# Kernel tuning notes

Measured on AMD Instinct MI355X. Metric: run time of the kernel, lower is better.

## Reference

```python
import jax, jax.numpy as jnp
import numpy as np

B, S, D = 1, 2048, 4096
H, KVH, HD = 32, 8, 128


def setup_inputs() -> dict:
    key = jax.random.key(0)
    ks = jax.random.split(key, 6)
    x = jax.random.normal(ks[0], (B, S, D), dtype=jnp.float32)
    # Llama3 RoPE angles: theta = 500000
    inv_freq = 1.0 / (500000.0 ** (np.arange(0, HD, 2, dtype=np.float32) / HD))
    ang = np.arange(S, dtype=np.float32)[:, None] * inv_freq[None, :]  # [S, HD//2]
    freqs_cos = jnp.asarray(np.cos(ang), dtype=jnp.float32)
    freqs_sin = jnp.asarray(np.sin(ang), dtype=jnp.float32)
    sc = 0.02
    wq = jax.random.normal(ks[1], (H * HD, D), dtype=jnp.float32) * sc
    wk = jax.random.normal(ks[2], (KVH * HD, D), dtype=jnp.float32) * sc
    wv = jax.random.normal(ks[3], (KVH * HD, D), dtype=jnp.float32) * sc
    wo = jax.random.normal(ks[4], (D, H * HD), dtype=jnp.float32) * sc
    return {"x": x, "freqs_cos": freqs_cos, "freqs_sin": freqs_sin,
            "wq": wq, "wk": wk, "wv": wv, "wo": wo}


def _rope(t, cos, sin):
    # t: [B, S, h, HD]; rotate consecutive pairs (complex multiply)
    t2 = t.reshape(*t.shape[:-1], HD // 2, 2)
    x0, x1 = t2[..., 0], t2[..., 1]
    c = cos[None, :, None, :]
    s = sin[None, :, None, :]
    r0 = x0 * c - x1 * s
    r1 = x0 * s + x1 * c
    return jnp.stack([r0, r1], axis=-1).reshape(t.shape)


def reference(x, freqs_cos, freqs_sin, wq, wk, wv, wo):
    b, s, _ = x.shape
    q = jnp.einsum('bsd,ed->bse', x, wq).reshape(b, s, H, HD)
    k = jnp.einsum('bsd,ed->bse', x, wk).reshape(b, s, KVH, HD)
    v = jnp.einsum('bsd,ed->bse', x, wv).reshape(b, s, KVH, HD)
    q = _rope(q, freqs_cos, freqs_sin)
    k = _rope(k, freqs_cos, freqs_sin)
    # GQA: repeat kv heads
    rep = H // KVH
    k = jnp.repeat(k, rep, axis=2)
    v = jnp.repeat(v, rep, axis=2)
    scale = 1.0 / jnp.sqrt(jnp.asarray(HD, dtype=x.dtype))
    scores = jnp.einsum('bqhd,bkhd->bhqk', q, k) * scale
    causal = jnp.tril(jnp.ones((s, s), dtype=bool))
    scores = jnp.where(causal[None, None], scores, jnp.finfo(scores.dtype).min)
    p = jax.nn.softmax(scores, axis=-1)
    out = jnp.einsum('bhqk,bkhd->bqhd', p, v).reshape(b, s, H * HD)
    return jnp.einsum('bse,de->bsd', out, wo)
```

## Files before the change

kernel.cpp:

```cpp
#include <hip/hip_runtime.h>

typedef unsigned short u16;
typedef short bf16x8 __attribute__((ext_vector_type(8)));
typedef float f32x4 __attribute__((ext_vector_type(4)));

#define S_LEN 2048
#define ATT_SCALE (0.08838834764831845f * 1.4426950408889634f)
#define NEG_BIG  -1.0e30f

static __device__ __forceinline__ float bf2f(u16 u) {
  union { unsigned int i; float f; } v; v.i = ((unsigned int)u) << 16; return v.f;
}
static __device__ __forceinline__ u16 f2bf(float f) {
  union { float f; unsigned int i; } v; v.f = f;
  unsigned int x = v.i;
  return (u16)((x + 0x7fffu + ((x >> 16) & 1u)) >> 16);
}
static __device__ __forceinline__ float fexp2(float x) {
  return __builtin_amdgcn_exp2f(x);
}

static __device__ __forceinline__ void gl_lds16(const u16* g, u16* l) {
  __builtin_amdgcn_global_load_lds(
      (const __attribute__((address_space(1))) unsigned int*)g,
      (__attribute__((address_space(3))) unsigned int*)l, 16, 0, 0);
}

static __device__ __forceinline__ bf16x8 load8(const u16* p) { return *(const bf16x8*)p; }
static __device__ __forceinline__ bf16x8 load8(const float* p) {
  f32x4 a = *(const f32x4*)p;
  f32x4 b = *(const f32x4*)(p + 4);
  bf16x8 r;
  r[0] = (short)f2bf(a[0]); r[1] = (short)f2bf(a[1]);
  r[2] = (short)f2bf(a[2]); r[3] = (short)f2bf(a[3]);
  r[4] = (short)f2bf(b[0]); r[5] = (short)f2bf(b[1]);
  r[6] = (short)f2bf(b[2]); r[7] = (short)f2bf(b[3]);
  return r;
}
static __device__ __forceinline__ void store_out(u16* C, size_t i, float v)  { C[i] = f2bf(v); }
static __device__ __forceinline__ void store_out(float* C, size_t i, float v){ C[i] = v; }

__global__ __launch_bounds__(256) void f2b_kernel(
    const float* __restrict__ s, u16* __restrict__ d, int n8) {
  int i = blockIdx.x * 256 + threadIdx.x;
  if (i >= n8) return;
  *(bf16x8*)&d[(size_t)i * 8] = load8(s + (size_t)i * 8);
}

template <typename OT>
static __device__ __forceinline__ void gemm_core(
    const u16* __restrict__ A, const u16* __restrict__ B, OT* __restrict__ C,
    int K, int ldc, int bm, int bn) {
  __shared__ __align__(16) u16 As[128 * 64];
  __shared__ __align__(16) u16 Bs[128 * 64];
  const int tid  = threadIdx.x;
  const int lane = tid & 63;
  const int wave = tid >> 6;
  const int wm = (wave >> 1) << 6;
  const int wn = (wave & 1) << 6;
  const int col  = lane & 15;
  const int quad = lane >> 4;

  const f32x4 fzero = {0.f, 0.f, 0.f, 0.f};
  f32x4 acc[4][4];
#pragma unroll
  for (int i = 0; i < 4; ++i)
#pragma unroll
    for (int j = 0; j < 4; ++j) acc[i][j] = fzero;

  const int srow = (lane >> 3);
  const int sc8  = lane & 7;

  for (int k0 = 0; k0 < K; k0 += 64) {
#pragma unroll
    for (int i = 0; i < 4; ++i) {
      int r = wave * 32 + i * 8 + srow;
      int src = (sc8 ^ (r & 7)) << 3;
      gl_lds16(A + (size_t)(bm + r) * K + k0 + src, &As[(wave * 32 + i * 8) * 64]);
      gl_lds16(B + (size_t)(bn + r) * K + k0 + src, &Bs[(wave * 32 + i * 8) * 64]);
    }
    __syncthreads();
#pragma unroll
    for (int kk = 0; kk < 64; kk += 32) {
      bf16x8 af[4], bfr[4];
#pragma unroll
      for (int mt = 0; mt < 4; ++mt) {
        int row = wm + mt * 16 + col;
        af[mt] = *(const bf16x8*)&As[row * 64 + ((((kk >> 3) + quad) ^ (col & 7)) << 3)];
      }
#pragma unroll
      for (int nt = 0; nt < 4; ++nt) {
        int row = wn + nt * 16 + col;
        bfr[nt] = *(const bf16x8*)&Bs[row * 64 + ((((kk >> 3) + quad) ^ (col & 7)) << 3)];
      }
#pragma unroll
      for (int mt = 0; mt < 4; ++mt)
#pragma unroll
        for (int nt = 0; nt < 4; ++nt)
          acc[mt][nt] = __builtin_amdgcn_mfma_f32_16x16x32_bf16(
              af[mt], bfr[nt], acc[mt][nt], 0, 0, 0);
    }
    __syncthreads();
  }
#pragma unroll
  for (int mt = 0; mt < 4; ++mt)
#pragma unroll
    for (int nt = 0; nt < 4; ++nt)
#pragma unroll
      for (int r = 0; r < 4; ++r) {
        int row = bm + wm + mt * 16 + quad * 4 + r;
        int cn  = bn + wn + nt * 16 + col;
        store_out(C, (size_t)row * ldc + cn, acc[mt][nt][r]);
      }
}

__global__ __launch_bounds__(256) void gemm_qkv(
    const u16* __restrict__ xb, const u16* __restrict__ wqb,
    const u16* __restrict__ wkb, const u16* __restrict__ wvb,
    u16* __restrict__ q, u16* __restrict__ k, u16* __restrict__ v) {
  int bx = blockIdx.x;
  const u16* B; u16* C; int ldc, bn;
  if (bx < 32)      { B = wqb; C = q; ldc = 4096; bn = bx * 128; }
  else if (bx < 40) { B = wkb; C = k; ldc = 1024; bn = (bx - 32) * 128; }
  else              { B = wvb; C = v; ldc = 1024; bn = (bx - 40) * 128; }
  gemm_core<u16>(xb, B, C, 4096, ldc, blockIdx.y * 128, bn);
}

__global__ __launch_bounds__(256) void gemm_o(
    const u16* __restrict__ ao, const u16* __restrict__ wob, float* __restrict__ out) {
  gemm_core<float>(ao, wob, out, 4096, 4096, blockIdx.y * 128, blockIdx.x * 128);
}

#define LDK 72
template <typename AT, typename BT, typename OT>
__global__ __launch_bounds__(256) void gemm_bt(
    const AT* __restrict__ A, const BT* __restrict__ B,
    OT* __restrict__ C, int M, int N, int K) {
  __shared__ __align__(16) u16 As[128 * LDK];
  __shared__ __align__(16) u16 Bs[128 * LDK];
  const int tid  = threadIdx.x;
  const int lane = tid & 63;
  const int wave = tid >> 6;
  const int wm = (wave >> 1) << 6;
  const int wn = (wave & 1) << 6;
  const int col  = lane & 15;
  const int quad = lane >> 4;
  const int bm = blockIdx.y * 128;
  const int bn = blockIdx.x * 128;

  const f32x4 fzero = {0.f, 0.f, 0.f, 0.f};
  f32x4 acc[4][4];
#pragma unroll
  for (int i = 0; i < 4; ++i)
#pragma unroll
    for (int j = 0; j < 4; ++j) acc[i][j] = fzero;

  const int sr = tid >> 3;
  const int sc = (tid & 7) * 8;
  const AT* Aptr = A + (size_t)(bm + sr) * K + sc;
  const BT* Bptr = B + (size_t)(bn + sr) * K + sc;

  for (int k0 = 0; k0 < K; k0 += 64) {
#pragma unroll
    for (int p = 0; p < 4; ++p) {
      *(bf16x8*)&As[(sr + 32 * p) * LDK + sc] = load8(Aptr + (size_t)(32 * p) * K + k0);
      *(bf16x8*)&Bs[(sr + 32 * p) * LDK + sc] = load8(Bptr + (size_t)(32 * p) * K + k0);
    }
    __syncthreads();
#pragma unroll
    for (int kk = 0; kk < 64; kk += 32) {
      bf16x8 af[4], bfr[4];
#pragma unroll
      for (int mt = 0; mt < 4; ++mt)
        af[mt] = *(const bf16x8*)&As[(wm + mt * 16 + col) * LDK + kk + quad * 8];
#pragma unroll
      for (int nt = 0; nt < 4; ++nt)
        bfr[nt] = *(const bf16x8*)&Bs[(wn + nt * 16 + col) * LDK + kk + quad * 8];
#pragma unroll
      for (int mt = 0; mt < 4; ++mt)
#pragma unroll
        for (int nt = 0; nt < 4; ++nt)
          acc[mt][nt] = __builtin_amdgcn_mfma_f32_16x16x32_bf16(
              af[mt], bfr[nt], acc[mt][nt], 0, 0, 0);
    }
    __syncthreads();
  }
#pragma unroll
  for (int mt = 0; mt < 4; ++mt)
#pragma unroll
    for (int nt = 0; nt < 4; ++nt)
#pragma unroll
      for (int r = 0; r < 4; ++r) {
        int row = bm + wm + mt * 16 + quad * 4 + r;
        int cn  = bn + wn + nt * 16 + col;
        store_out(C, (size_t)row * N + cn, acc[mt][nt][r]);
      }
}

__global__ __launch_bounds__(256) void rope_kernel(
    u16* __restrict__ q, u16* __restrict__ k,
    const float* __restrict__ cs, const float* __restrict__ sn) {
  int idx = blockIdx.x * 256 + threadIdx.x;
  const int QP = S_LEN * 32 * 64;
  u16* base;
  int s, i;
  bool isq = idx < QP;
  if (isq) {
    s = idx >> 11; int w = idx & 2047; i = w & 63;
    base = q + (size_t)s * 4096 + (w >> 6) * 128 + 2 * i;
  } else {
    int j = idx - QP;
    s = j >> 9; int w = j & 511; i = w & 63;
    base = k + (size_t)s * 1024 + (w >> 6) * 128 + 2 * i;
  }
  float c  = cs[s * 64 + i];
  float sv = sn[s * 64 + i];
  float x0 = bf2f(base[0]);
  float x1 = bf2f(base[1]);
  float r0 = x0 * c - x1 * sv;
  float r1 = x0 * sv + x1 * c;
  if (isq) { r0 *= ATT_SCALE; r1 *= ATT_SCALE; }
  base[0] = f2bf(r0);
  base[1] = f2bf(r1);
}

__global__ __launch_bounds__(512, 4) void attn_kernel(
    const u16* __restrict__ Q, const u16* __restrict__ K,
    const u16* __restrict__ V, u16* __restrict__ O) {
  const int ib   = blockIdx.x;
  const int h    = blockIdx.y;
  const int kvh  = h >> 2;
  const int tid  = threadIdx.x;
  const int lane = tid & 63;
  const int wave = tid >> 6;
  const int grp  = wave >> 2;
  const int wl   = wave & 3;
  const int col  = lane & 15;
  const int quad = lane >> 4;
  const int gt   = tid & 255;

  __shared__ __align__(16) u16 SMEM[2][16384];
  u16* Kb = &SMEM[grp][0];
  u16* Vb = &SMEM[grp][8192];

  const f32x4 fzero = {0.f, 0.f, 0.f, 0.f};

  const int krow = lane >> 4;
  const int kcnk = lane & 15;
  const int vsc  = (gt & 15) * 8;
  const int vrp  = gt >> 4;
  const int vrot = gt & 7;

  for (int t = 0; t < 2; ++t) {
    const int qb   = t ? 31 - ib : ib;
    const int qpos = qb * 64 + wl * 16 + col;
    const int ql   = wl * 16 + col;

    bf16x8 qf[4];
#pragma unroll
    for (int kb = 0; kb < 4; ++kb)
      qf[kb] = *(const bf16x8*)&Q[(size_t)qpos * 4096 + h * 128 + kb * 32 + quad * 8];

    f32x4 oacc[8];
#pragma unroll
    for (int nt = 0; nt < 8; ++nt) oacc[nt] = fzero;
    float m_ = NEG_BIG, l_ = 0.f;

    const int n  = qb + 1;
    const int h0 = (n + 1) >> 1;
    const int c0 = grp ? h0 : 0;
    const int c1 = grp ? n  : h0;

    for (int rnd = 0; rnd < h0; ++rnd) {
      const int c = c0 + rnd;
      const bool act = c < c1;
      if (act) {
        const int pos0 = c * 64;
#pragma unroll
        for (int i = 0; i < 4; ++i) {
          int r = wl * 16 + i * 4 + krow;
          int src = ((kcnk & 8) | ((kcnk ^ r) & 7)) << 3;
          gl_lds16(&K[(size_t)(pos0 + r) * 1024 + kvh * 128 + src],
                   &Kb[(wl * 16 + i * 4) * 128]);
        }
#pragma unroll
        for (int it = 0; it < 2; ++it) {
          int rp = vrp + it * 16;
          const u16* vp = &V[(size_t)(pos0 + 2 * rp) * 1024 + kvh * 128 + vsc];
          union { bf16x8 v; u16 u[8]; } ue, uo;
          ue.v = *(const bf16x8*)vp;
          uo.v = *(const bf16x8*)(vp + 1024);
          int pc = rp >> 2, pi = rp & 3;
#pragma unroll
          for (int j = 0; j < 8; ++j) {
            int jj = (j + vrot) & 7;
            int hd = vsc + jj;
            unsigned val = (unsigned)ue.u[jj] | ((unsigned)uo.u[jj] << 16);
            *(unsigned*)&Vb[hd * 64 + ((pc ^ (hd & 7)) << 3) + pi * 2] = val;
          }
        }
      }
      __syncthreads();
      if (act) {
        const int pos0 = c * 64;
        const bool diag = (c == qb);

        f32x4 sv[4];
#pragma unroll
        for (int kv = 0; kv < 4; ++kv) sv[kv] = fzero;
        __builtin_amdgcn_s_setprio(1);
#pragma unroll
        for (int kv = 0; kv < 4; ++kv) {
          int r = kv * 16 + col;
#pragma unroll
          for (int kb = 0; kb < 4; ++kb) {
            int kq = kb * 4 + quad;
            int slot = (kq & 8) | ((kq ^ r) & 7);
            bf16x8 kf = *(const bf16x8*)&Kb[r * 128 + slot * 8];
            sv[kv] = __builtin_amdgcn_mfma_f32_16x16x32_bf16(kf, qf[kb], sv[kv], 0, 0, 0);
          }
        }
        __builtin_amdgcn_s_setprio(0);

        float mx = NEG_BIG;
        if (diag) {
#pragma unroll
          for (int kv = 0; kv < 4; ++kv)
#pragma unroll
            for (int r = 0; r < 4; ++r) {
              float s = (pos0 + kv * 16 + quad * 4 + r) <= qpos ? sv[kv][r] : NEG_BIG;
              sv[kv][r] = s;
              mx = fmaxf(mx, s);
            }
        } else {
#pragma unroll
          for (int kv = 0; kv < 4; ++kv)
#pragma unroll
            for (int r = 0; r < 4; ++r) mx = fmaxf(mx, sv[kv][r]);
        }
        mx = fmaxf(mx, __shfl_xor(mx, 16));
        mx = fmaxf(mx, __shfl_xor(mx, 32));
        if (!__all(mx - m_ <= 8.f)) {
          float mnew  = fmaxf(m_, mx);
          float alpha = fexp2(m_ - mnew);
          l_ *= alpha;
#pragma unroll
          for (int nt = 0; nt < 8; ++nt) {
            oacc[nt][0] *= alpha; oacc[nt][1] *= alpha;
            oacc[nt][2] *= alpha; oacc[nt][3] *= alpha;
          }
          m_ = mnew;
        }
        float ls = 0.f;
#pragma unroll
        for (int kv = 0; kv < 4; ++kv)
#pragma unroll
          for (int r = 0; r < 4; ++r) {
            float p = fexp2(sv[kv][r] - m_);
            sv[kv][r] = p;
            ls += p;
          }
        ls += __shfl_xor(ls, 16);
        ls += __shfl_xor(ls, 32);
        l_ += ls;

        unsigned pk[4][2];
#pragma unroll
        for (int kv = 0; kv < 4; ++kv) {
          pk[kv][0] = (unsigned)f2bf(sv[kv][0]) | ((unsigned)f2bf(sv[kv][1]) << 16);
          pk[kv][1] = (unsigned)f2bf(sv[kv][2]) | ((unsigned)f2bf(sv[kv][3]) << 16);
        }

        const int idxA = col + 16 * (2 * (quad & 1));
        const int idxB = idxA + 16;
        const bool hi  = quad >= 2;
#pragma unroll
        for (int kc = 0; kc < 2; ++kc) {
          unsigned a00 = __shfl(pk[2 * kc][0],     idxA);
          unsigned a01 = __shfl(pk[2 * kc][1],     idxA);
          unsigned a10 = __shfl(pk[2 * kc + 1][0], idxA);
          unsigned a11 = __shfl(pk[2 * kc + 1][1], idxA);
          unsigned b00 = __shfl(pk[2 * kc][0],     idxB);
          unsigned b01 = __shfl(pk[2 * kc][1],     idxB);
          unsigned b10 = __shfl(pk[2 * kc + 1][0], idxB);
          unsigned b11 = __shfl(pk[2 * kc + 1][1], idxB);
          union { unsigned u[4]; bf16x8 v; } pb;
          pb.u[0] = hi ? a10 : a00;
          pb.u[1] = hi ? a11 : a01;
          pb.u[2] = hi ? b10 : b00;
          pb.u[3] = hi ? b11 : b01;
          __builtin_amdgcn_s_setprio(1);
#pragma unroll
          for (int nt = 0; nt < 8; ++nt) {
            int hd = nt * 16 + col;
            int pc = kc * 4 + quad;
            bf16x8 vf = *(const bf16x8*)&Vb[hd * 64 + ((pc ^ (hd & 7)) << 3)];
            oacc[nt] = __builtin_amdgcn_mfma_f32_16x16x32_bf16(vf, pb.v, oacc[nt], 0, 0, 0);
          }
          __builtin_amdgcn_s_setprio(0);
        }
      }
      __syncthreads();
    }

    float* MF = (float*)&SMEM[0][0];
    float* ML = MF + 64 * 132;
    if (grp == 1) {
#pragma unroll
      for (int nt = 0; nt < 8; ++nt)
        *(f32x4*)&MF[ql * 132 + nt * 16 + quad * 4] = oacc[nt];
      if (quad == 0) { ML[2 * ql] = m_; ML[2 * ql + 1] = l_; }
    }
    __syncthreads();
    if (grp == 0) {
      float m1 = ML[2 * ql], l1 = ML[2 * ql + 1];
      float mn = fmaxf(m_, m1);
      float a0 = fexp2(m_ - mn), a1 = fexp2(m1 - mn);
      float li = 1.f / (l_ * a0 + l1 * a1);
      a0 *= li; a1 *= li;
#pragma unroll
      for (int nt = 0; nt < 8; ++nt) {
        f32x4 o1 = *(const f32x4*)&MF[ql * 132 + nt * 16 + quad * 4];
        union { u16 u[4]; unsigned long long ll; } w;
        w.u[0] = f2bf(oacc[nt][0] * a0 + o1[0] * a1);
        w.u[1] = f2bf(oacc[nt][1] * a0 + o1[1] * a1);
        w.u[2] = f2bf(oacc[nt][2] * a0 + o1[2] * a1);
        w.u[3] = f2bf(oacc[nt][3] * a0 + o1[3] * a1);
        *(unsigned long long*)&O[(size_t)qpos * 4096 + h * 128 + nt * 16 + quad * 4] = w.ll;
      }
    }
    __syncthreads();
  }
}

extern "C" void kernel_launch(void* const* d_in, const int* in_sizes, int n_in,
                              void* d_out, int out_size, void* d_ws, size_t ws_size,
                              hipStream_t stream) {
  const float* x  = (const float*)d_in[0];
  const float* fc = (const float*)d_in[1];
  const float* fs = (const float*)d_in[2];
  const float* wq = (const float*)d_in[3];
  const float* wk = (const float*)d_in[4];
  const float* wv = (const float*)d_in[5];
  const float* wo = (const float*)d_in[6];
  float* out = (float*)d_out;

  u16* q  = (u16*)d_ws;
  u16* k  = q + (size_t)8388608;
  u16* v  = k + (size_t)2097152;
  u16* ao = v + (size_t)2097152;

  dim3 blk(256, 1, 1);
  dim3 ablk(512, 1, 1);
  const size_t NEED_FAST = 109051904ULL;

  if (ws_size >= NEED_FAST) {
    u16* xb  = ao  + (size_t)8388608;
    u16* wqb = xb  + (size_t)8388608;
    u16* wkb = wqb + (size_t)16777216;
    u16* wvb = wkb + (size_t)4194304;
    u16* wob = wqb;

    hipLaunchKernelGGL(f2b_kernel, dim3(4096, 1, 1), blk, 0, stream, x,  xb,  1048576);
    hipLaunchKernelGGL(f2b_kernel, dim3(8192, 1, 1), blk, 0, stream, wq, wqb, 2097152);
    hipLaunchKernelGGL(f2b_kernel, dim3(2048, 1, 1), blk, 0, stream, wk, wkb, 524288);
    hipLaunchKernelGGL(f2b_kernel, dim3(2048, 1, 1), blk, 0, stream, wv, wvb, 524288);
    hipLaunchKernelGGL(gemm_qkv, dim3(48, 16, 1), blk, 0, stream, xb, wqb, wkb, wvb, q, k, v);
    hipLaunchKernelGGL(f2b_kernel, dim3(8192, 1, 1), blk, 0, stream, wo, wob, 2097152);
    hipLaunchKernelGGL(rope_kernel, dim3(20480, 1, 1), blk, 0, stream, q, k, fc, fs);
    hipLaunchKernelGGL(attn_kernel, dim3(16, 32, 1), ablk, 0, stream, q, k, v, ao);
    hipLaunchKernelGGL(gemm_o, dim3(32, 16, 1), blk, 0, stream, ao, wob, out);
  } else {
    hipLaunchKernelGGL((gemm_bt<float, float, u16>), dim3(32, 16, 1), blk, 0, stream,
                       x, wq, q, 2048, 4096, 4096);
    hipLaunchKernelGGL((gemm_bt<float, float, u16>), dim3(8, 16, 1),  blk, 0, stream,
                       x, wk, k, 2048, 1024, 4096);
    hipLaunchKernelGGL((gemm_bt<float, float, u16>), dim3(8, 16, 1),  blk, 0, stream,
                       x, wv, v, 2048, 1024, 4096);
    hipLaunchKernelGGL(rope_kernel, dim3(20480, 1, 1), blk, 0, stream, q, k, fc, fs);
    hipLaunchKernelGGL(attn_kernel, dim3(16, 32, 1), ablk, 0, stream, q, k, v, ao);
    hipLaunchKernelGGL((gemm_bt<u16, float, float>), dim3(32, 16, 1), blk, 0, stream,
                       ao, wo, out, 2048, 4096, 4096);
  }
}
```

Before: 542.4 us.

## Enlarge attention query tile to 128 rows per block with two subtiles per wave

Each attention block now handles 128 query rows, with each wave holding two 16-row query subtiles, so every K/V fragment loaded from LDS feeds two MFMAs. The grid halves to 8x32 and the two wave groups split the key range evenly, which removes the idle inactive rounds of the old uneven split. The LDS swizzle is changed and a separate stat buffer is added for the merge step. The aim is to cut LDS traffic and K/V reloads per FLOP, at the cost of doubled accumulator registers (launch bounds lowered to 2), fewer blocks, and masking applied to more tiles.

```diff
diff --git a/kernel.cpp b/kernel.cpp
--- a/kernel.cpp
+++ b/kernel.cpp
@@ -224,7 +224,7 @@
   base[1] = f2bf(r1);
 }
 
-__global__ __launch_bounds__(512, 4) void attn_kernel(
+__global__ __launch_bounds__(512, 2) void attn_kernel(
     const u16* __restrict__ Q, const u16* __restrict__ K,
     const u16* __restrict__ V, u16* __restrict__ O) {
   const int ib   = blockIdx.x;
@@ -237,9 +237,11 @@
   const int wl   = wave & 3;
   const int col  = lane & 15;
   const int quad = lane >> 4;
+  const int chd  = col >> 3;
   const int gt   = tid & 255;
 
   __shared__ __align__(16) u16 SMEM[2][16384];
+  __shared__ float MLS[256];
   u16* Kb = &SMEM[grp][0];
   u16* Vb = &SMEM[grp][8192];
 
@@ -252,181 +254,213 @@
   const int vrot = gt & 7;
 
   for (int t = 0; t < 2; ++t) {
-    const int qb   = t ? 31 - ib : ib;
-    const int qpos = qb * 64 + wl * 16 + col;
-    const int ql   = wl * 16 + col;
-
-    bf16x8 qf[4];
-#pragma unroll
-    for (int kb = 0; kb < 4; ++kb)
-      qf[kb] = *(const bf16x8*)&Q[(size_t)qpos * 4096 + h * 128 + kb * 32 + quad * 8];
-
-    f32x4 oacc[8];
-#pragma unroll
-    for (int nt = 0; nt < 8; ++nt) oacc[nt] = fzero;
-    float m_ = NEG_BIG, l_ = 0.f;
-
-    const int n  = qb + 1;
-    const int h0 = (n + 1) >> 1;
-    const int c0 = grp ? h0 : 0;
-    const int c1 = grp ? n  : h0;
-
-    for (int rnd = 0; rnd < h0; ++rnd) {
-      const int c = c0 + rnd;
-      const bool act = c < c1;
-      if (act) {
-        const int pos0 = c * 64;
-#pragma unroll
-        for (int i = 0; i < 4; ++i) {
-          int r = wl * 16 + i * 4 + krow;
-          int src = ((kcnk & 8) | ((kcnk ^ r) & 7)) << 3;
-          gl_lds16(&K[(size_t)(pos0 + r) * 1024 + kvh * 128 + src],
-                   &Kb[(wl * 16 + i * 4) * 128]);
-        }
-#pragma unroll
-        for (int it = 0; it < 2; ++it) {
-          int rp = vrp + it * 16;
-          const u16* vp = &V[(size_t)(pos0 + 2 * rp) * 1024 + kvh * 128 + vsc];
-          union { bf16x8 v; u16 u[8]; } ue, uo;
-          ue.v = *(const bf16x8*)vp;
-          uo.v = *(const bf16x8*)(vp + 1024);
-          int pc = rp >> 2, pi = rp & 3;
-#pragma unroll
-          for (int j = 0; j < 8; ++j) {
-            int jj = (j + vrot) & 7;
-            int hd = vsc + jj;
-            unsigned val = (unsigned)ue.u[jj] | ((unsigned)uo.u[jj] << 16);
-            *(unsigned*)&Vb[hd * 64 + ((pc ^ (hd & 7)) << 3) + pi * 2] = val;
-          }
+    const int qb = t ? 15 - ib : ib;
+    const int rb = qb * 128 + wl * 32;
+
+    bf16x8 qf[2][4];
+#pragma unroll
+    for (int u = 0; u < 2; ++u)
+#pragma unroll
+      for (int kb = 0; kb < 4; ++kb)
+        qf[u][kb] = *(const bf16x8*)&Q[(size_t)(rb + u * 16 + col) * 4096 +
+                                       h * 128 + kb * 32 + quad * 8];
+
+    f32x4 oacc[2][8];
+#pragma unroll
+    for (int u = 0; u < 2; ++u)
+#pragma unroll
+      for (int nt = 0; nt < 8; ++nt) oacc[u][nt] = fzero;
+    float m_[2] = {NEG_BIG, NEG_BIG};
+    float l_[2] = {0.f, 0.f};
+
+    const int nr = qb + 1;
+    for (int rnd = 0; rnd < nr; ++rnd) {
+      const int c    = grp * nr + rnd;
+      const int pos0 = c * 64;
+
+#pragma unroll
+      for (int i = 0; i < 4; ++i) {
+        int r  = wl * 16 + i * 4 + krow;
+        int g  = (kcnk & 8) |
+                 ((((kcnk ^ r) & 7) + (((r >> 3) & 1) << 2)) & 7);
+        gl_lds16(&K[(size_t)(pos0 + r) * 1024 + kvh * 128 + g * 8],
+                 &Kb[(wl * 16 + i * 4) * 128]);
+      }
+#pragma unroll
+      for (int it = 0; it < 2; ++it) {
+        int rp = vrp + it * 16;
+        const u16* vp = &V[(size_t)(pos0 + 2 * rp) * 1024 + kvh * 128 + vsc];
+        union { bf16x8 v; u16 u[8]; } ue, uo;
+        ue.v = *(const bf16x8*)vp;
+        uo.v = *(const bf16x8*)(vp + 1024);
+        int pc = rp >> 2, pi = rp & 3;
+#pragma unroll
+        for (int j = 0; j < 8; ++j) {
+          int jj = (j + vrot) & 7;
+          int hd = vsc + jj;
+          int swz = (((pc + (((hd >> 3) & 1) << 2)) & 7) ^ (hd & 7));
+          unsigned val = (unsigned)ue.u[jj] | ((unsigned)uo.u[jj] << 16);
+          *(unsigned*)&Vb[hd * 64 + swz * 8 + pi * 2] = val;
         }
       }
       __syncthreads();
-      if (act) {
-        const int pos0 = c * 64;
-        const bool diag = (c == qb);
-
-        f32x4 sv[4];
-#pragma unroll
-        for (int kv = 0; kv < 4; ++kv) sv[kv] = fzero;
-        __builtin_amdgcn_s_setprio(1);
-#pragma unroll
-        for (int kv = 0; kv < 4; ++kv) {
-          int r = kv * 16 + col;
-#pragma unroll
-          for (int kb = 0; kb < 4; ++kb) {
-            int kq = kb * 4 + quad;
-            int slot = (kq & 8) | ((kq ^ r) & 7);
-            bf16x8 kf = *(const bf16x8*)&Kb[r * 128 + slot * 8];
-            sv[kv] = __builtin_amdgcn_mfma_f32_16x16x32_bf16(kf, qf[kb], sv[kv], 0, 0, 0);
-          }
-        }
-        __builtin_amdgcn_s_setprio(0);
-
+
+      f32x4 sv[2][4];
+#pragma unroll
+      for (int u = 0; u < 2; ++u)
+#pragma unroll
+        for (int kv = 0; kv < 4; ++kv) sv[u][kv] = fzero;
+      __builtin_amdgcn_s_setprio(1);
+#pragma unroll
+      for (int kv = 0; kv < 4; ++kv) {
+        int r = kv * 16 + col;
+#pragma unroll
+        for (int kb = 0; kb < 4; ++kb) {
+          int kq   = kb * 4 + quad;
+          int slot = (kq & 8) | ((((kq & 7) + (chd << 2)) & 7) ^ (r & 7));
+          bf16x8 kf = *(const bf16x8*)&Kb[r * 128 + slot * 8];
+          sv[0][kv] = __builtin_amdgcn_mfma_f32_16x16x32_bf16(kf, qf[0][kv*0+kb], sv[0][kv], 0, 0, 0);
+          sv[1][kv] = __builtin_amdgcn_mfma_f32_16x16x32_bf16(kf, qf[1][kb], sv[1][kv], 0, 0, 0);
+        }
+      }
+      __builtin_amdgcn_s_setprio(0);
+
+      unsigned pk[2][4][2];
+#pragma unroll
+      for (int u = 0; u < 2; ++u) {
+        const int ubase = rb + u * 16;
+        const int qpos  = ubase + col;
+        const bool nomask = (pos0 + 63 <= ubase);
         float mx = NEG_BIG;
-        if (diag) {
+        if (nomask) {
 #pragma unroll
           for (int kv = 0; kv < 4; ++kv)
 #pragma unroll
+            for (int r = 0; r < 4; ++r) mx = fmaxf(mx, sv[u][kv][r]);
+        } else {
+#pragma unroll
+          for (int kv = 0; kv < 4; ++kv)
+#pragma unroll
             for (int r = 0; r < 4; ++r) {
-              float s = (pos0 + kv * 16 + quad * 4 + r) <= qpos ? sv[kv][r] : NEG_BIG;
-              sv[kv][r] = s;
+              bool keep = (pos0 + kv * 16 + quad * 4 + r) <= qpos;
+              float s = keep ? sv[u][kv][r] : NEG_BIG;
+              sv[u][kv][r] = s;
               mx = fmaxf(mx, s);
             }
-        } else {
-#pragma unroll
-          for (int kv = 0; kv < 4; ++kv)
-#pragma unroll
-            for (int r = 0; r < 4; ++r) mx = fmaxf(mx, sv[kv][r]);
         }
         mx = fmaxf(mx, __shfl_xor(mx, 16));
         mx = fmaxf(mx, __shfl_xor(mx, 32));
-        if (!__all(mx - m_ <= 8.f)) {
-          float mnew  = fmaxf(m_, mx);
-          float alpha = fexp2(m_ - mnew);
-          l_ *= alpha;
+        if (!__all(mx - m_[u] <= 8.f)) {
+          float mnew  = fmaxf(m_[u], mx);
+          float alpha = fexp2(m_[u] - mnew);
+          l_[u] *= alpha;
 #pragma unroll
           for (int nt = 0; nt < 8; ++nt) {
-            oacc[nt][0] *= alpha; oacc[nt][1] *= alpha;
-            oacc[nt][2] *= alpha; oacc[nt][3] *= alpha;
+            oacc[u][nt][0] *= alpha; oacc[u][nt][1] *= alpha;
+            oacc[u][nt][2] *= alpha; oacc[u][nt][3] *= alpha;
           }
-          m_ = mnew;
+          m_[u] = mnew;
         }
         float ls = 0.f;
-#pragma unroll
-        for (int kv = 0; kv < 4; ++kv)
-#pragma unroll
-          for (int r = 0; r < 4; ++r) {
-            float p = fexp2(sv[kv][r] - m_);
-            sv[kv][r] = p;
-            ls += p;
-          }
+        if (nomask) {
+#pragma unroll
+          for (int kv = 0; kv < 4; ++kv)
+#pragma unroll
+            for (int r = 0; r < 4; ++r) {
+              float p = fexp2(sv[u][kv][r] - m_[u]);
+              sv[u][kv][r] = p;
+              ls += p;
+            }
+        } else {
+#pragma unroll
+          for (int kv = 0; kv < 4; ++kv)
+#pragma unroll
+            for (int r = 0; r < 4; ++r) {
+              float p = fexp2(sv[u][kv][r] - m_[u]);
+              bool keep = (pos0 + kv * 16 + quad * 4 + r) <= qpos;
+              p = keep ? p : 0.f;
+              sv[u][kv][r] = p;
+              ls += p;
+            }
+        }
         ls += __shfl_xor(ls, 16);
         ls += __shfl_xor(ls, 32);
-        l_ += ls;
-
-        unsigned pk[4][2];
+        l_[u] += ls;
 #pragma unroll
         for (int kv = 0; kv < 4; ++kv) {
-          pk[kv][0] = (unsigned)f2bf(sv[kv][0]) | ((unsigned)f2bf(sv[kv][1]) << 16);
-          pk[kv][1] = (unsigned)f2bf(sv[kv][2]) | ((unsigned)f2bf(sv[kv][3]) << 16);
-        }
-
-        const int idxA = col + 16 * (2 * (quad & 1));
-        const int idxB = idxA + 16;
-        const bool hi  = quad >= 2;
-#pragma unroll
-        for (int kc = 0; kc < 2; ++kc) {
-          unsigned a00 = __shfl(pk[2 * kc][0],     idxA);
-          unsigned a01 = __shfl(pk[2 * kc][1],     idxA);
-          unsigned a10 = __shfl(pk[2 * kc + 1][0], idxA);
-          unsigned a11 = __shfl(pk[2 * kc + 1][1], idxA);
-          unsigned b00 = __shfl(pk[2 * kc][0],     idxB);
-          unsigned b01 = __shfl(pk[2 * kc][1],     idxB);
-          unsigned b10 = __shfl(pk[2 * kc + 1][0], idxB);
-          unsigned b11 = __shfl(pk[2 * kc + 1][1], idxB);
-          union { unsigned u[4]; bf16x8 v; } pb;
-          pb.u[0] = hi ? a10 : a00;
-          pb.u[1] = hi ? a11 : a01;
-          pb.u[2] = hi ? b10 : b00;
-          pb.u[3] = hi ? b11 : b01;
-          __builtin_amdgcn_s_setprio(1);
-#pragma unroll
-          for (int nt = 0; nt < 8; ++nt) {
-            int hd = nt * 16 + col;
-            int pc = kc * 4 + quad;
-            bf16x8 vf = *(const bf16x8*)&Vb[hd * 64 + ((pc ^ (hd & 7)) << 3)];
-            oacc[nt] = __builtin_amdgcn_mfma_f32_16x16x32_bf16(vf, pb.v, oacc[nt], 0, 0, 0);
-          }
-          __builtin_amdgcn_s_setprio(0);
-        }
+          pk[u][kv][0] = (unsigned)f2bf(sv[u][kv][0]) | ((unsigned)f2bf(sv[u][kv][1]) << 16);
+          pk[u][kv][1] = (unsigned)f2bf(sv[u][kv][2]) | ((unsigned)f2bf(sv[u][kv][3]) << 16);
+        }
+      }
+
+      const int idxA = col + 16 * (2 * (quad & 1));
+      const int idxB = idxA + 16;
+      const bool hi  = quad >= 2;
+#pragma unroll
+      for (int kc = 0; kc < 2; ++kc) {
+        union { unsigned u[4]; bf16x8 v; } pb[2];
+#pragma unroll
+        for (int u = 0; u < 2; ++u) {
+          unsigned a00 = __shfl(pk[u][2 * kc][0],     idxA);
+          unsigned a01 = __shfl(pk[u][2 * kc][1],     idxA);
+          unsigned a10 = __shfl(pk[u][2 * kc + 1][0], idxA);
+          unsigned a11 = __shfl(pk[u][2 * kc + 1][1], idxA);
+          unsigned b00 = __shfl(pk[u][2 * kc][0],     idxB);
+          unsigned b01 = __shfl(pk[u][2 * kc][1],     idxB);
+          unsigned b10 = __shfl(pk[u][2 * kc + 1][0], idxB);
+          unsigned b11 = __shfl(pk[u][2 * kc + 1][1], idxB);
+          pb[u].u[0] = hi ? a10 : a00;
+          pb[u].u[1] = hi ? a11 : a01;
+          pb[u].u[2] = hi ? b10 : b00;
+          pb[u].u[3] = hi ? b11 : b01;
+        }
+        __builtin_amdgcn_s_setprio(1);
+#pragma unroll
+        for (int nt = 0; nt < 8; ++nt) {
+          int hd  = nt * 16 + col;
+          int pc  = kc * 4 + quad;
+          int swz = (((pc + (chd << 2)) & 7) ^ (hd & 7));
+          bf16x8 vf = *(const bf16x8*)&Vb[hd * 64 + swz * 8];
+          oacc[0][nt] = __builtin_amdgcn_mfma_f32_16x16x32_bf16(vf, pb[0].v, oacc[0][nt], 0, 0, 0);
+          oacc[1][nt] = __builtin_amdgcn_mfma_f32_16x16x32_bf16(vf, pb[1].v, oacc[1][nt], 0, 0, 0);
+        }
+        __builtin_amdgcn_s_setprio(0);
       }
       __syncthreads();
     }
 
     float* MF = (float*)&SMEM[0][0];
-    float* ML = MF + 64 * 132;
     if (grp == 1) {
 #pragma unroll
-      for (int nt = 0; nt < 8; ++nt)
-        *(f32x4*)&MF[ql * 132 + nt * 16 + quad * 4] = oacc[nt];
-      if (quad == 0) { ML[2 * ql] = m_; ML[2 * ql + 1] = l_; }
+      for (int u = 0; u < 2; ++u) {
+        int ql = wl * 32 + u * 16 + col;
+#pragma unroll
+        for (int nt = 0; nt < 8; ++nt)
+          *(f32x4*)&MF[(size_t)ql * 128 + nt * 16 + quad * 4] = oacc[u][nt];
+        if (quad == 0) { MLS[2 * ql] = m_[u]; MLS[2 * ql + 1] = l_[u]; }
+      }
     }
     __syncthreads();
     if (grp == 0) {
-      float m1 = ML[2 * ql], l1 = ML[2 * ql + 1];
-      float mn = fmaxf(m_, m1);
-      float a0 = fexp2(m_ - mn), a1 = fexp2(m1 - mn);
-      float li = 1.f / (l_ * a0 + l1 * a1);
-      a0 *= li; a1 *= li;
-#pragma unroll
-      for (int nt = 0; nt < 8; ++nt) {
-        f32x4 o1 = *(const f32x4*)&MF[ql * 132 + nt * 16 + quad * 4];
-        union { u16 u[4]; unsigned long long ll; } w;
-        w.u[0] = f2bf(oacc[nt][0] * a0 + o1[0] * a1);
-        w.u[1] = f2bf(oacc[nt][1] * a0 + o1[1] * a1);
-        w.u[2] = f2bf(oacc[nt][2] * a0 + o1[2] * a1);
-        w.u[3] = f2bf(oacc[nt][3] * a0 + o1[3] * a1);
-        *(unsigned long long*)&O[(size_t)qpos * 4096 + h * 128 + nt * 16 + quad * 4] = w.ll;
+#pragma unroll
+      for (int u = 0; u < 2; ++u) {
+        int ql = wl * 32 + u * 16 + col;
+        int qpos = qb * 128 + ql;
+        float m1 = MLS[2 * ql], l1 = MLS[2 * ql + 1];
+        float mn = fmaxf(m_[u], m1);
+        float a0 = fexp2(m_[u] - mn), a1 = fexp2(m1 - mn);
+        float li = 1.f / (l_[u] * a0 + l1 * a1);
+        a0 *= li; a1 *= li;
+#pragma unroll
+        for (int nt = 0; nt < 8; ++nt) {
+          f32x4 o1 = *(const f32x4*)&MF[(size_t)ql * 128 + nt * 16 + quad * 4];
+          union { u16 u[4]; unsigned long long ll; } w;
+          w.u[0] = f2bf(oacc[u][nt][0] * a0 + o1[0] * a1);
+          w.u[1] = f2bf(oacc[u][nt][1] * a0 + o1[1] * a1);
+          w.u[2] = f2bf(oacc[u][nt][2] * a0 + o1[2] * a1);
+          w.u[3] = f2bf(oacc[u][nt][3] * a0 + o1[3] * a1);
+          *(unsigned long long*)&O[(size_t)qpos * 4096 + h * 128 + nt * 16 + quad * 4] = w.ll;
+        }
       }
     }
     __syncthreads();
@@ -468,7 +502,7 @@
     hipLaunchKernelGGL(gemm_qkv, dim3(48, 16, 1), blk, 0, stream, xb, wqb, wkb, wvb, q, k, v);
     hipLaunchKernelGGL(f2b_kernel, dim3(8192, 1, 1), blk, 0, stream, wo, wob, 2097152);
     hipLaunchKernelGGL(rope_kernel, dim3(20480, 1, 1), blk, 0, stream, q, k, fc, fs);
-    hipLaunchKernelGGL(attn_kernel, dim3(16, 32, 1), ablk, 0, stream, q, k, v, ao);
+    hipLaunchKernelGGL(attn_kernel, dim3(8, 32, 1), ablk, 0, stream, q, k, v, ao);
     hipLaunchKernelGGL(gemm_o, dim3(32, 16, 1), blk, 0, stream, ao, wob, out);
   } else {
     hipLaunchKernelGGL((gemm_bt<float, float, u16>), dim3(32, 16, 1), blk, 0, stream,
@@ -478,7 +512,7 @@
     hipLaunchKernelGGL((gemm_bt<float, float, u16>), dim3(8, 16, 1),  blk, 0, stream,
                        x, wv, v, 2048, 1024, 4096);
     hipLaunchKernelGGL(rope_kernel, dim3(20480, 1, 1), blk, 0, stream, q, k, fc, fs);
-    hipLaunchKernelGGL(attn_kernel, dim3(16, 32, 1), ablk, 0, stream, q, k, v, ao);
+    hipLaunchKernelGGL(attn_kernel, dim3(8, 32, 1), ablk, 0, stream, q, k, v, ao);
     hipLaunchKernelGGL((gemm_bt<u16, float, float>), dim3(32, 16, 1), blk, 0, stream,
                        ao, wo, out, 2048, 4096, 4096);
   }
```

Result: no change. 537.5 us (-0.9%).
